# Kernel optimization log

Hardware: AMD Instinct MI355X
Metric: run time of the kernel (lower is better)

The kernel has to match this reference:

```python
import math
import jax, jax.numpy as jnp
import numpy as np

N_HEADS = 32
N_KV_HEADS = 8
HEAD_DIM = 128
DIM = 4096
B = 32
MAX_SEQ = 4096
Q_LEN = 1
START_POS = 4095


def setup_inputs() -> dict:
    key = jax.random.key(0)
    ks = jax.random.split(key, 9)
    x = jax.random.normal(ks[0], (B, Q_LEN, DIM), dtype=jnp.float32)
    # RoPE angles for the current positions (seqlen=Q_LEN, half head_dim pairs)
    inv_freq = 1.0 / (500000.0 ** (np.arange(0, HEAD_DIM, 2, dtype=np.float32) / HEAD_DIM))
    pos = np.arange(START_POS, START_POS + Q_LEN, dtype=np.float32)
    ang = pos[:, None] * inv_freq[None, :]  # [Q_LEN, HEAD_DIM//2]
    freqs_cos = jnp.asarray(np.cos(ang), dtype=jnp.float32)
    freqs_sin = jnp.asarray(np.sin(ang), dtype=jnp.float32)
    cache_k = jax.random.normal(ks[1], (B, MAX_SEQ, N_KV_HEADS, HEAD_DIM), dtype=jnp.float32)
    cache_v = jax.random.normal(ks[2], (B, MAX_SEQ, N_KV_HEADS, HEAD_DIM), dtype=jnp.float32)
    s = 0.02
    wq = jax.random.normal(ks[3], (N_HEADS * HEAD_DIM, DIM), dtype=jnp.float32) * s
    wk = jax.random.normal(ks[4], (N_KV_HEADS * HEAD_DIM, DIM), dtype=jnp.float32) * s
    wv = jax.random.normal(ks[5], (N_KV_HEADS * HEAD_DIM, DIM), dtype=jnp.float32) * s
    wo = jax.random.normal(ks[6], (DIM, N_HEADS * HEAD_DIM), dtype=jnp.float32) * s
    return {"x": x, "start_pos": START_POS, "freqs_cos": freqs_cos, "freqs_sin": freqs_sin,
            "cache_k": cache_k, "cache_v": cache_v, "wq": wq, "wk": wk, "wv": wv, "wo": wo}


def _rope(t, cos, sin):
    # t: [B, S, h, hd]; cos/sin: [S, hd//2]; complex multiply on (even, odd) pairs
    tr = t.reshape(*t.shape[:-1], HEAD_DIM // 2, 2)
    a, b = tr[..., 0], tr[..., 1]
    c = cos[None, :, None, :]
    s = sin[None, :, None, :]
    out = jnp.stack([a * c - b * s, a * s + b * c], axis=-1)
    return out.reshape(t.shape)


def reference(x, start_pos, freqs_cos, freqs_sin, cache_k, cache_v, wq, wk, wv, wo):
    bsz, seqlen, _ = x.shape
    n_rep = N_HEADS // N_KV_HEADS
    xq = jnp.einsum('bsd,od->bso', x, wq).reshape(bsz, seqlen, N_HEADS, HEAD_DIM)
    xk = jnp.einsum('bsd,od->bso', x, wk).reshape(bsz, seqlen, N_KV_HEADS, HEAD_DIM)
    xv = jnp.einsum('bsd,od->bso', x, wv).reshape(bsz, seqlen, N_KV_HEADS, HEAD_DIM)
    xq = _rope(xq, freqs_cos, freqs_sin)
    xk = _rope(xk, freqs_cos, freqs_sin)
    # KV-cache update (start_pos is a static Python int)
    cache_k = cache_k.at[:, start_pos:start_pos + seqlen].set(xk)
    cache_v = cache_v.at[:, start_pos:start_pos + seqlen].set(xv)
    keys = cache_k[:, :start_pos + seqlen]    # [B, T, Hkv, hd]
    values = cache_v[:, :start_pos + seqlen]  # [B, T, Hkv, hd]
    # GQA: group query heads [H] -> [Hkv, n_rep]; avoids materializing repeated KV
    q = xq.reshape(bsz, seqlen, N_KV_HEADS, n_rep, HEAD_DIM)
    scale = 1.0 / math.sqrt(HEAD_DIM)
    scores = jnp.einsum('bsgrd,btgd->bgrst', q, keys) * scale  # [B, Hkv, n_rep, S, T]
    probs = jax.nn.softmax(scores, axis=-1)
    out = jnp.einsum('bgrst,btgd->bsgrd', probs, values)
    out = out.reshape(bsz, seqlen, N_HEADS * HEAD_DIM)
    return jnp.einsum('bse,de->bsd', out, wo)
```

## Files before the change

kernel.cpp:

```cpp
#include <hip/hip_runtime.h>

#define B_    32
#define DIM_  4096
#define NH_   32
#define NKV_  8
#define HD_   128
#define TSEQ  4096
#define NQKV  6144
#define GSPLIT 32
#define BK    32
#define NT    256
#define TSPL  8
#define TS    512

__device__ __forceinline__ const float* wrow(const float* w0, const float* w1,
                                             const float* w2, int b1, int b2, int col) {
    if (col < b1) return w0 + (size_t)col * DIM_;
    if (col < b2) return w1 + (size_t)(col - b1) * DIM_;
    return w2 + (size_t)(col - b2) * DIM_;
}

__global__ __launch_bounds__(128) void gemm32(
    const float* __restrict__ A, const float* __restrict__ w0,
    const float* __restrict__ w1, const float* __restrict__ w2,
    int b1, int b2, int N, float* __restrict__ po)
{
    __shared__ __align__(16) float wt[BK][NT + 4];
    __shared__ __align__(16) float xs[BK][36];
    const int tid = threadIdx.x;
    const int cg  = tid & 31;
    const int bg  = tid >> 5;
    const int ct  = blockIdx.x * NT;
    const int k0  = blockIdx.y * (DIM_ / GSPLIT);

    float acc[8][8];
    #pragma unroll
    for (int i = 0; i < 8; ++i)
        #pragma unroll
        for (int j = 0; j < 8; ++j) acc[i][j] = 0.f;

    const int kq = (tid & 7) * 4;
    const int rr = tid >> 3;

    for (int kt = 0; kt < DIM_ / GSPLIT; kt += BK) {
        const int kb = k0 + kt;
        #pragma unroll
        for (int st = 0; st < 16; ++st) {
            const int c = st * 16 + rr;
            const float* wr = wrow(w0, w1, w2, b1, b2, ct + c);
            const float4 wv = *(const float4*)(wr + kb + kq);
            wt[kq + 0][c] = wv.x; wt[kq + 1][c] = wv.y;
            wt[kq + 2][c] = wv.z; wt[kq + 3][c] = wv.w;
        }
        #pragma unroll
        for (int st = 0; st < 2; ++st) {
            const int b = st * 16 + rr;
            const float4 xv = *(const float4*)(A + (size_t)b * DIM_ + kb + kq);
            xs[kq + 0][b] = xv.x; xs[kq + 1][b] = xv.y;
            xs[kq + 2][b] = xv.z; xs[kq + 3][b] = xv.w;
        }
        __syncthreads();
        #pragma unroll 8
        for (int kk = 0; kk < BK; ++kk) {
            const float4 xa = *(const float4*)&xs[kk][bg * 8];
            const float4 xb = *(const float4*)&xs[kk][bg * 8 + 4];
            const float4 wa = *(const float4*)&wt[kk][cg * 4];
            const float4 wb = *(const float4*)&wt[kk][128 + cg * 4];
            const float xv[8] = {xa.x, xa.y, xa.z, xa.w, xb.x, xb.y, xb.z, xb.w};
            const float wv[8] = {wa.x, wa.y, wa.z, wa.w, wb.x, wb.y, wb.z, wb.w};
            #pragma unroll
            for (int i = 0; i < 8; ++i)
                #pragma unroll
                for (int j = 0; j < 8; ++j)
                    acc[i][j] = fmaf(xv[i], wv[j], acc[i][j]);
        }
        __syncthreads();
    }
    const size_t srow = (size_t)blockIdx.y * B_;
    #pragma unroll
    for (int i = 0; i < 8; ++i) {
        const int b = bg * 8 + i;
        const float4 o0 = make_float4(acc[i][0], acc[i][1], acc[i][2], acc[i][3]);
        const float4 o1 = make_float4(acc[i][4], acc[i][5], acc[i][6], acc[i][7]);
        *(float4*)&po[(srow + b) * N + ct + cg * 4]       = o0;
        *(float4*)&po[(srow + b) * N + ct + 128 + cg * 4] = o1;
    }
}

__global__ void reduce_rope(const float* __restrict__ po,
                            const float* __restrict__ fc, const float* __restrict__ fs,
                            float* __restrict__ qkv)
{
    const int pid = blockIdx.x * 256 + threadIdx.x;
    const int b  = pid / 3072;
    const int c0 = (pid - b * 3072) * 2;
    float v0 = 0.f, v1 = 0.f;
    #pragma unroll
    for (int s = 0; s < GSPLIT; ++s) {
        const float* p = po + ((size_t)s * B_ + b) * NQKV + c0;
        v0 += p[0]; v1 += p[1];
    }
    if (c0 < DIM_ + NKV_ * HD_) {
        const int i = (c0 & 127) >> 1;
        const float c = fc[i], sn = fs[i];
        const float o0 = v0 * c - v1 * sn;
        const float o1 = v0 * sn + v1 * c;
        v0 = o0; v1 = o1;
    }
    qkv[(size_t)b * NQKV + c0]     = v0;
    qkv[(size_t)b * NQKV + c0 + 1] = v1;
}

__global__ __launch_bounds__(256) void attn_partial(
    const float* __restrict__ qkv, const float* __restrict__ ck,
    const float* __restrict__ cv,
    float* __restrict__ po , float* __restrict__ pl )
{
    const int blk = blockIdx.x;
    const int s = blk & (TSPL - 1);
    const int g = (blk / TSPL) & 7;
    const int b = blk / (TSPL * NKV_);
    const int tid    = threadIdx.x;
    const int grp    = tid >> 4;
    const int lane16 = tid & 15;
    const int wv     = tid >> 6;
    const int g4     = (tid >> 4) & 3;
    const int d8     = lane16 * 8;
    const float* qb = qkv + (size_t)b * NQKV;

    float4 qa[4], qc[4];
    #pragma unroll
    for (int h = 0; h < 4; ++h) {
        qa[h] = *(const float4*)(qb + (g * 4 + h) * HD_ + d8);
        qc[h] = *(const float4*)(qb + (g * 4 + h) * HD_ + d8 + 4);
    }

    float acc[4][8];
    #pragma unroll
    for (int h = 0; h < 4; ++h)
        #pragma unroll
        for (int e = 0; e < 8; ++e) acc[h][e] = 0.f;
    float l[4] = {0.f, 0.f, 0.f, 0.f};
    const float scale = 0.08838834764831845f;
    const int t0 = s * TS + grp;

    for (int it = 0; it < TS / 16; ++it) {
        const int t = t0 + it * 16;
        const float *kp, *vp;
        if (t == TSEQ - 1) {
            kp = qb + DIM_ + g * HD_;
            vp = qb + DIM_ + NKV_ * HD_ + g * HD_;
        } else {
            const size_t off = (((size_t)b * TSEQ + t) * NKV_ + g) * HD_;
            kp = ck + off; vp = cv + off;
        }
        const float4 k0 = *(const float4*)(kp + d8);
        const float4 k1 = *(const float4*)(kp + d8 + 4);
        float p[4];
        #pragma unroll
        for (int h = 0; h < 4; ++h) {
            p[h] = k0.x*qa[h].x + k0.y*qa[h].y + k0.z*qa[h].z + k0.w*qa[h].w
                 + k1.x*qc[h].x + k1.y*qc[h].y + k1.z*qc[h].z + k1.w*qc[h].w;
        }
        #pragma unroll
        for (int off = 1; off < 16; off <<= 1) {
            #pragma unroll
            for (int h = 0; h < 4; ++h) p[h] += __shfl_xor(p[h], off);
        }
        #pragma unroll
        for (int h = 0; h < 4; ++h) {
            p[h] = __expf(p[h] * scale);
            l[h] += p[h];
        }
        const float4 v0 = *(const float4*)(vp + d8);
        const float4 v1 = *(const float4*)(vp + d8 + 4);
        #pragma unroll
        for (int h = 0; h < 4; ++h) {
            acc[h][0] += p[h]*v0.x; acc[h][1] += p[h]*v0.y;
            acc[h][2] += p[h]*v0.z; acc[h][3] += p[h]*v0.w;
            acc[h][4] += p[h]*v1.x; acc[h][5] += p[h]*v1.y;
            acc[h][6] += p[h]*v1.z; acc[h][7] += p[h]*v1.w;
        }
    }

    #pragma unroll
    for (int off = 16; off < 64; off <<= 1) {
        #pragma unroll
        for (int h = 0; h < 4; ++h) {
            #pragma unroll
            for (int e = 0; e < 8; ++e) acc[h][e] += __shfl_xor(acc[h][e], off);
            l[h] += __shfl_xor(l[h], off);
        }
    }

    __shared__ __align__(16) float ob[4][4][HD_];
    __shared__ float lb[4][4];
    if (g4 == 0) {
        #pragma unroll
        for (int h = 0; h < 4; ++h)
            #pragma unroll
            for (int e = 0; e < 8; ++e) ob[wv][h][d8 + e] = acc[h][e];
        if (lane16 == 0) {
            #pragma unroll
            for (int h = 0; h < 4; ++h) lb[wv][h] = l[h];
        }
    }
    __syncthreads();
    #pragma unroll
    for (int e = tid; e < 512; e += 256) {
        float sum = 0.f;
        #pragma unroll
        for (int c = 0; c < 4; ++c) sum += ob[c][e >> 7][e & 127];
        po[(size_t)blk * 512 + e] = sum;
    }
    if (tid < 4) {
        float sum = 0.f;
        #pragma unroll
        for (int c = 0; c < 4; ++c) sum += lb[c][tid];
        pl[blk * 4 + tid] = sum;
    }
}

__global__ void attn_combine(const float* __restrict__ po, const float* __restrict__ pl,
                             float* __restrict__ ao)
{
    const int bg  = blockIdx.x;
    const int tid = threadIdx.x;
    const int e0  = tid * 4;
    const int r   = e0 >> 7;
    float4 o = make_float4(0.f, 0.f, 0.f, 0.f);
    float ls = 0.f;
    #pragma unroll
    for (int s = 0; s < TSPL; ++s) {
        const float4 v = *(const float4*)&po[((size_t)bg * TSPL + s) * 512 + e0];
        o.x += v.x; o.y += v.y; o.z += v.z; o.w += v.w;
        ls += pl[(bg * TSPL + s) * 4 + r];
    }
    const float inv = 1.f / ls;
    o.x *= inv; o.y *= inv; o.z *= inv; o.w *= inv;
    const int b = bg >> 3, g = bg & 7;
    *(float4*)&ao[(size_t)b * DIM_ + g * 512 + e0] = o;
}

__global__ void reduce_out(const float* __restrict__ po, float* __restrict__ out)
{
    const int i = blockIdx.x * 256 + threadIdx.x;
    const int b = i >> 12, c = i & 4095;
    float v = 0.f;
    #pragma unroll
    for (int s = 0; s < GSPLIT; ++s) v += po[((size_t)s * B_ + b) * DIM_ + c];
    out[i] = v;
}

extern "C" void kernel_launch(void* const* d_in, const int* in_sizes, int n_in,
                              void* d_out, int out_size, void* d_ws, size_t ws_size,
                              hipStream_t stream)
{
    (void)in_sizes; (void)n_in; (void)out_size; (void)ws_size;
    const float* x  = (const float*)d_in[0];
    const float* fc = (const float*)d_in[2];
    const float* fs = (const float*)d_in[3];
    const float* ck = (const float*)d_in[4];
    const float* cv = (const float*)d_in[5];
    const float* wq = (const float*)d_in[6];
    const float* wk = (const float*)d_in[7];
    const float* wv = (const float*)d_in[8];
    const float* wo = (const float*)d_in[9];
    float* out = (float*)d_out;
    float* ws  = (float*)d_ws;

    float* qkv  = ws;
    float* aout = ws + 196608;
    float* apo  = ws + 327680;
    float* apl  = ws + 1376256;
    float* gp   = ws + 1384448;

    gemm32<<<dim3(NQKV / NT, GSPLIT), 128, 0, stream>>>(
        x, wq, wk, wv, DIM_, DIM_ + NKV_ * HD_, NQKV, gp);
    reduce_rope<<<dim3((B_ * (NQKV / 2)) / 256), 256, 0, stream>>>(gp, fc, fs, qkv);
    attn_partial<<<dim3(B_ * NKV_ * TSPL), 256, 0, stream>>>(qkv, ck, cv, apo, apl);
    attn_combine<<<dim3(B_ * NKV_), 128, 0, stream>>>(apo, apl, aout);
    gemm32<<<dim3(DIM_ / NT, GSPLIT), 128, 0, stream>>>(
        aout, wo, wo, wo, DIM_, DIM_, DIM_, gp);
    reduce_out<<<dim3((B_ * DIM_) / 256), 256, 0, stream>>>(gp, out);
}
```

Baseline: 285.3 us.

## Prefetch weights into registers, nontemporal KV streaming, vectorize reductions

The split-K GEMM now stages its whole 128-wide slice of the activation once in shared memory. It register-prefetches the next weight tile with nontemporal loads while computing the current one, and picks the weight base pointer once per block. Attention switches to 32 lanes per key with one float4 each, software-pipelined nontemporal K/V loads, and no per-iteration branch for the fresh token. The reduce kernels use float4 loads and stores. The aim is better overlap of latency on the bandwidth-bound weight and KV-cache streams, at the cost of more registers and longer shuffle chains in attention.

New measurement: 268.6 us. 5.8% less time.

```diff
diff --git a/kernel.cpp b/kernel.cpp
--- a/kernel.cpp
+++ b/kernel.cpp
@@ -13,11 +13,10 @@
 #define TSPL  8
 #define TS    512
 
-__device__ __forceinline__ const float* wrow(const float* w0, const float* w1,
-                                             const float* w2, int b1, int b2, int col) {
-    if (col < b1) return w0 + (size_t)col * DIM_;
-    if (col < b2) return w1 + (size_t)(col - b1) * DIM_;
-    return w2 + (size_t)(col - b2) * DIM_;
+typedef float f4_t __attribute__((ext_vector_type(4)));
+
+__device__ __forceinline__ f4_t ntl(const float* p) {
+    return __builtin_nontemporal_load((const f4_t*)p);
 }
 
 __global__ __launch_bounds__(128) void gemm32(
@@ -26,48 +25,67 @@
     int b1, int b2, int N, float* __restrict__ po)
 {
     __shared__ __align__(16) float wt[BK][NT + 4];
-    __shared__ __align__(16) float xs[BK][36];
+    __shared__ __align__(16) float xp[128][36];
     const int tid = threadIdx.x;
     const int cg  = tid & 31;
     const int bg  = tid >> 5;
     const int ct  = blockIdx.x * NT;
     const int k0  = blockIdx.y * (DIM_ / GSPLIT);
 
+    const float* wb_; int c0_;
+    if (ct < b1)      { wb_ = w0; c0_ = ct; }
+    else if (ct < b2) { wb_ = w1; c0_ = ct - b1; }
+    else              { wb_ = w2; c0_ = ct - b2; }
+
+    {
+        const int kq = (tid & 31) * 4;
+        const int rr = tid >> 5;
+        #pragma unroll
+        for (int st = 0; st < 8; ++st) {
+            const int bb = st * 4 + rr;
+            const float4 xv = *(const float4*)(A + (size_t)bb * DIM_ + k0 + kq);
+            xp[kq + 0][bb] = xv.x; xp[kq + 1][bb] = xv.y;
+            xp[kq + 2][bb] = xv.z; xp[kq + 3][bb] = xv.w;
+        }
+    }
+
+    const int kq2 = (tid & 7) * 4;
+    const int rr2 = tid >> 3;
+    f4_t wreg[16];
+
+    #pragma unroll
+    for (int st = 0; st < 16; ++st)
+        wreg[st] = ntl(wb_ + (size_t)(c0_ + st * 16 + rr2) * DIM_ + k0 + kq2);
+    #pragma unroll
+    for (int st = 0; st < 16; ++st) {
+        const int c = st * 16 + rr2;
+        wt[kq2 + 0][c] = wreg[st][0]; wt[kq2 + 1][c] = wreg[st][1];
+        wt[kq2 + 2][c] = wreg[st][2]; wt[kq2 + 3][c] = wreg[st][3];
+    }
+    __syncthreads();
+
     float acc[8][8];
     #pragma unroll
     for (int i = 0; i < 8; ++i)
         #pragma unroll
         for (int j = 0; j < 8; ++j) acc[i][j] = 0.f;
 
-    const int kq = (tid & 7) * 4;
-    const int rr = tid >> 3;
-
-    for (int kt = 0; kt < DIM_ / GSPLIT; kt += BK) {
-        const int kb = k0 + kt;
-        #pragma unroll
-        for (int st = 0; st < 16; ++st) {
-            const int c = st * 16 + rr;
-            const float* wr = wrow(w0, w1, w2, b1, b2, ct + c);
-            const float4 wv = *(const float4*)(wr + kb + kq);
-            wt[kq + 0][c] = wv.x; wt[kq + 1][c] = wv.y;
-            wt[kq + 2][c] = wv.z; wt[kq + 3][c] = wv.w;
-        }
-        #pragma unroll
-        for (int st = 0; st < 2; ++st) {
-            const int b = st * 16 + rr;
-            const float4 xv = *(const float4*)(A + (size_t)b * DIM_ + kb + kq);
-            xs[kq + 0][b] = xv.x; xs[kq + 1][b] = xv.y;
-            xs[kq + 2][b] = xv.z; xs[kq + 3][b] = xv.w;
-        }
-        __syncthreads();
+    for (int t = 0; t < 4; ++t) {
+        if (t < 3) {
+            #pragma unroll
+            for (int st = 0; st < 16; ++st)
+                wreg[st] = ntl(wb_ + (size_t)(c0_ + st * 16 + rr2) * DIM_
+                               + k0 + (t + 1) * BK + kq2);
+        }
         #pragma unroll 8
         for (int kk = 0; kk < BK; ++kk) {
-            const float4 xa = *(const float4*)&xs[kk][bg * 8];
-            const float4 xb = *(const float4*)&xs[kk][bg * 8 + 4];
+            const int kr = t * BK + kk;
+            const float4 xa = *(const float4*)&xp[kr][bg * 8];
+            const float4 xb = *(const float4*)&xp[kr][bg * 8 + 4];
             const float4 wa = *(const float4*)&wt[kk][cg * 4];
-            const float4 wb = *(const float4*)&wt[kk][128 + cg * 4];
+            const float4 wb4 = *(const float4*)&wt[kk][128 + cg * 4];
             const float xv[8] = {xa.x, xa.y, xa.z, xa.w, xb.x, xb.y, xb.z, xb.w};
-            const float wv[8] = {wa.x, wa.y, wa.z, wa.w, wb.x, wb.y, wb.z, wb.w};
+            const float wv[8] = {wa.x, wa.y, wa.z, wa.w, wb4.x, wb4.y, wb4.z, wb4.w};
             #pragma unroll
             for (int i = 0; i < 8; ++i)
                 #pragma unroll
@@ -75,7 +93,17 @@
                     acc[i][j] = fmaf(xv[i], wv[j], acc[i][j]);
         }
         __syncthreads();
-    }
+        if (t < 3) {
+            #pragma unroll
+            for (int st = 0; st < 16; ++st) {
+                const int c = st * 16 + rr2;
+                wt[kq2 + 0][c] = wreg[st][0]; wt[kq2 + 1][c] = wreg[st][1];
+                wt[kq2 + 2][c] = wreg[st][2]; wt[kq2 + 3][c] = wreg[st][3];
+            }
+            __syncthreads();
+        }
+    }
+
     const size_t srow = (size_t)blockIdx.y * B_;
     #pragma unroll
     for (int i = 0; i < 8; ++i) {
@@ -92,23 +120,46 @@
                             float* __restrict__ qkv)
 {
     const int pid = blockIdx.x * 256 + threadIdx.x;
-    const int b  = pid / 3072;
-    const int c0 = (pid - b * 3072) * 2;
-    float v0 = 0.f, v1 = 0.f;
-    #pragma unroll
-    for (int s = 0; s < GSPLIT; ++s) {
-        const float* p = po + ((size_t)s * B_ + b) * NQKV + c0;
-        v0 += p[0]; v1 += p[1];
-    }
+    const int b  = pid / (NQKV / 4);
+    const int c0 = (pid - b * (NQKV / 4)) * 4;
+    f4_t v = {0.f, 0.f, 0.f, 0.f};
+    #pragma unroll
+    for (int s = 0; s < GSPLIT; ++s)
+        v += *(const f4_t*)(po + ((size_t)s * B_ + b) * NQKV + c0);
     if (c0 < DIM_ + NKV_ * HD_) {
         const int i = (c0 & 127) >> 1;
-        const float c = fc[i], sn = fs[i];
-        const float o0 = v0 * c - v1 * sn;
-        const float o1 = v0 * sn + v1 * c;
-        v0 = o0; v1 = o1;
-    }
-    qkv[(size_t)b * NQKV + c0]     = v0;
-    qkv[(size_t)b * NQKV + c0 + 1] = v1;
+        const float ca = fc[i],     sa = fs[i];
+        const float cb = fc[i + 1], sb = fs[i + 1];
+        f4_t o;
+        o[0] = v[0] * ca - v[1] * sa;
+        o[1] = v[0] * sa + v[1] * ca;
+        o[2] = v[2] * cb - v[3] * sb;
+        o[3] = v[2] * sb + v[3] * cb;
+        v = o;
+    }
+    *(f4_t*)(qkv + (size_t)b * NQKV + c0) = v;
+}
+
+__device__ __forceinline__ void attn_step(const f4_t kc, const f4_t vc,
+                                          const f4_t* q, f4_t* acc, float* l)
+{
+    float p0 = kc[0]*q[0][0] + kc[1]*q[0][1] + kc[2]*q[0][2] + kc[3]*q[0][3];
+    float p1 = kc[0]*q[1][0] + kc[1]*q[1][1] + kc[2]*q[1][2] + kc[3]*q[1][3];
+    float p2 = kc[0]*q[2][0] + kc[1]*q[2][1] + kc[2]*q[2][2] + kc[3]*q[2][3];
+    float p3 = kc[0]*q[3][0] + kc[1]*q[3][1] + kc[2]*q[3][2] + kc[3]*q[3][3];
+    #pragma unroll
+    for (int off = 1; off < 32; off <<= 1) {
+        p0 += __shfl_xor(p0, off);
+        p1 += __shfl_xor(p1, off);
+        p2 += __shfl_xor(p2, off);
+        p3 += __shfl_xor(p3, off);
+    }
+    const float scale = 0.08838834764831845f;
+    p0 = __expf(p0 * scale); p1 = __expf(p1 * scale);
+    p2 = __expf(p2 * scale); p3 = __expf(p3 * scale);
+    l[0] += p0; l[1] += p1; l[2] += p2; l[3] += p3;
+    acc[0] += p0 * vc; acc[1] += p1 * vc;
+    acc[2] += p2 * vc; acc[3] += p3 * vc;
 }
 
 __global__ __launch_bounds__(256) void attn_partial(
@@ -120,105 +171,72 @@
     const int s = blk & (TSPL - 1);
     const int g = (blk / TSPL) & 7;
     const int b = blk / (TSPL * NKV_);
-    const int tid    = threadIdx.x;
-    const int grp    = tid >> 4;
-    const int lane16 = tid & 15;
-    const int wv     = tid >> 6;
-    const int g4     = (tid >> 4) & 3;
-    const int d8     = lane16 * 8;
+    const int tid  = threadIdx.x;
+    const int grp  = tid >> 5;
+    const int lane = tid & 31;
+    const int wv   = tid >> 6;
+    const int d4   = lane * 4;
     const float* qb = qkv + (size_t)b * NQKV;
 
-    float4 qa[4], qc[4];
+    f4_t q[4];
+    #pragma unroll
+    for (int h = 0; h < 4; ++h)
+        q[h] = *(const f4_t*)(qb + (g * 4 + h) * HD_ + d4);
+
+    f4_t zero4 = {0.f, 0.f, 0.f, 0.f};
+    f4_t acc[4] = {zero4, zero4, zero4, zero4};
+    float l[4] = {0.f, 0.f, 0.f, 0.f};
+
+    const int t0 = s * TS + grp;
+    int niter = TS / 8;
+    const bool fresh = (s == TSPL - 1) && (grp == 7);
+    if (fresh) --niter;
+
+    const size_t base = (((size_t)b * TSEQ + t0) * NKV_ + g) * HD_ + d4;
+    const float* kp = ck + base;
+    const float* vp = cv + base;
+    const size_t step = (size_t)8 * NKV_ * HD_;
+
+    f4_t kc = ntl(kp), vc = ntl(vp);
+    for (int it = 0; it < niter - 1; ++it) {
+        kp += step; vp += step;
+        const f4_t kn = ntl(kp);
+        const f4_t vn = ntl(vp);
+        attn_step(kc, vc, q, acc, l);
+        kc = kn; vc = vn;
+    }
+    attn_step(kc, vc, q, acc, l);
+    if (fresh) {
+        const f4_t kf = *(const f4_t*)(qb + DIM_ + g * HD_ + d4);
+        const f4_t vf = *(const f4_t*)(qb + DIM_ + NKV_ * HD_ + g * HD_ + d4);
+        attn_step(kf, vf, q, acc, l);
+    }
+
     #pragma unroll
     for (int h = 0; h < 4; ++h) {
-        qa[h] = *(const float4*)(qb + (g * 4 + h) * HD_ + d8);
-        qc[h] = *(const float4*)(qb + (g * 4 + h) * HD_ + d8 + 4);
-    }
-
-    float acc[4][8];
-    #pragma unroll
-    for (int h = 0; h < 4; ++h)
         #pragma unroll
-        for (int e = 0; e < 8; ++e) acc[h][e] = 0.f;
-    float l[4] = {0.f, 0.f, 0.f, 0.f};
-    const float scale = 0.08838834764831845f;
-    const int t0 = s * TS + grp;
-
-    for (int it = 0; it < TS / 16; ++it) {
-        const int t = t0 + it * 16;
-        const float *kp, *vp;
-        if (t == TSEQ - 1) {
-            kp = qb + DIM_ + g * HD_;
-            vp = qb + DIM_ + NKV_ * HD_ + g * HD_;
-        } else {
-            const size_t off = (((size_t)b * TSEQ + t) * NKV_ + g) * HD_;
-            kp = ck + off; vp = cv + off;
-        }
-        const float4 k0 = *(const float4*)(kp + d8);
-        const float4 k1 = *(const float4*)(kp + d8 + 4);
-        float p[4];
-        #pragma unroll
-        for (int h = 0; h < 4; ++h) {
-            p[h] = k0.x*qa[h].x + k0.y*qa[h].y + k0.z*qa[h].z + k0.w*qa[h].w
-                 + k1.x*qc[h].x + k1.y*qc[h].y + k1.z*qc[h].z + k1.w*qc[h].w;
-        }
-        #pragma unroll
-        for (int off = 1; off < 16; off <<= 1) {
-            #pragma unroll
-            for (int h = 0; h < 4; ++h) p[h] += __shfl_xor(p[h], off);
-        }
-        #pragma unroll
-        for (int h = 0; h < 4; ++h) {
-            p[h] = __expf(p[h] * scale);
-            l[h] += p[h];
-        }
-        const float4 v0 = *(const float4*)(vp + d8);
-        const float4 v1 = *(const float4*)(vp + d8 + 4);
-        #pragma unroll
-        for (int h = 0; h < 4; ++h) {
-            acc[h][0] += p[h]*v0.x; acc[h][1] += p[h]*v0.y;
-            acc[h][2] += p[h]*v0.z; acc[h][3] += p[h]*v0.w;
-            acc[h][4] += p[h]*v1.x; acc[h][5] += p[h]*v1.y;
-            acc[h][6] += p[h]*v1.z; acc[h][7] += p[h]*v1.w;
-        }
-    }
-
-    #pragma unroll
-    for (int off = 16; off < 64; off <<= 1) {
-        #pragma unroll
-        for (int h = 0; h < 4; ++h) {
-            #pragma unroll
-            for (int e = 0; e < 8; ++e) acc[h][e] += __shfl_xor(acc[h][e], off);
-            l[h] += __shfl_xor(l[h], off);
-        }
+        for (int e = 0; e < 4; ++e) acc[h][e] += __shfl_xor(acc[h][e], 32);
+        l[h] += __shfl_xor(l[h], 32);
     }
 
     __shared__ __align__(16) float ob[4][4][HD_];
     __shared__ float lb[4][4];
-    if (g4 == 0) {
+    if ((tid & 32) == 0) {
         #pragma unroll
-        for (int h = 0; h < 4; ++h)
-            #pragma unroll
-            for (int e = 0; e < 8; ++e) ob[wv][h][d8 + e] = acc[h][e];
-        if (lane16 == 0) {
-            #pragma unroll
-            for (int h = 0; h < 4; ++h) lb[wv][h] = l[h];
+        for (int h = 0; h < 4; ++h) *(f4_t*)&ob[wv][h][d4] = acc[h];
+        if (lane == 0) {
+            lb[wv][0] = l[0]; lb[wv][1] = l[1]; lb[wv][2] = l[2]; lb[wv][3] = l[3];
         }
     }
     __syncthreads();
     #pragma unroll
     for (int e = tid; e < 512; e += 256) {
-        float sum = 0.f;
-        #pragma unroll
-        for (int c = 0; c < 4; ++c) sum += ob[c][e >> 7][e & 127];
+        const float sum = ob[0][e >> 7][e & 127] + ob[1][e >> 7][e & 127]
+                        + ob[2][e >> 7][e & 127] + ob[3][e >> 7][e & 127];
         po[(size_t)blk * 512 + e] = sum;
     }
-    if (tid < 4) {
-        float sum = 0.f;
-        #pragma unroll
-        for (int c = 0; c < 4; ++c) sum += lb[c][tid];
-        pl[blk * 4 + tid] = sum;
-    }
+    if (tid < 4)
+        pl[blk * 4 + tid] = lb[0][tid] + lb[1][tid] + lb[2][tid] + lb[3][tid];
 }
 
 __global__ void attn_combine(const float* __restrict__ po, const float* __restrict__ pl,
@@ -228,28 +246,28 @@
     const int tid = threadIdx.x;
     const int e0  = tid * 4;
     const int r   = e0 >> 7;
-    float4 o = make_float4(0.f, 0.f, 0.f, 0.f);
+    f4_t o = {0.f, 0.f, 0.f, 0.f};
     float ls = 0.f;
     #pragma unroll
     for (int s = 0; s < TSPL; ++s) {
-        const float4 v = *(const float4*)&po[((size_t)bg * TSPL + s) * 512 + e0];
-        o.x += v.x; o.y += v.y; o.z += v.z; o.w += v.w;
+        o += *(const f4_t*)&po[((size_t)bg * TSPL + s) * 512 + e0];
         ls += pl[(bg * TSPL + s) * 4 + r];
     }
-    const float inv = 1.f / ls;
-    o.x *= inv; o.y *= inv; o.z *= inv; o.w *= inv;
+    o *= (1.f / ls);
     const int b = bg >> 3, g = bg & 7;
-    *(float4*)&ao[(size_t)b * DIM_ + g * 512 + e0] = o;
+    *(f4_t*)&ao[(size_t)b * DIM_ + g * 512 + e0] = o;
 }
 
 __global__ void reduce_out(const float* __restrict__ po, float* __restrict__ out)
 {
-    const int i = blockIdx.x * 256 + threadIdx.x;
-    const int b = i >> 12, c = i & 4095;
-    float v = 0.f;
-    #pragma unroll
-    for (int s = 0; s < GSPLIT; ++s) v += po[((size_t)s * B_ + b) * DIM_ + c];
-    out[i] = v;
+    const int pid = blockIdx.x * 256 + threadIdx.x;
+    const int b  = pid >> 10;
+    const int c0 = (pid & 1023) * 4;
+    f4_t v = {0.f, 0.f, 0.f, 0.f};
+    #pragma unroll
+    for (int s = 0; s < GSPLIT; ++s)
+        v += *(const f4_t*)(po + ((size_t)s * B_ + b) * DIM_ + c0);
+    *(f4_t*)(out + (size_t)b * DIM_ + c0) = v;
 }
 
 extern "C" void kernel_launch(void* const* d_in, const int* in_sizes, int n_in,
@@ -277,10 +295,10 @@
 
     gemm32<<<dim3(NQKV / NT, GSPLIT), 128, 0, stream>>>(
         x, wq, wk, wv, DIM_, DIM_ + NKV_ * HD_, NQKV, gp);
-    reduce_rope<<<dim3((B_ * (NQKV / 2)) / 256), 256, 0, stream>>>(gp, fc, fs, qkv);
+    reduce_rope<<<dim3(B_ * (NQKV / 4) / 256), 256, 0, stream>>>(gp, fc, fs, qkv);
     attn_partial<<<dim3(B_ * NKV_ * TSPL), 256, 0, stream>>>(qkv, ck, cv, apo, apl);
     attn_combine<<<dim3(B_ * NKV_), 128, 0, stream>>>(apo, apl, aout);
     gemm32<<<dim3(DIM_ / NT, GSPLIT), 128, 0, stream>>>(
         aout, wo, wo, wo, DIM_, DIM_, DIM_, gp);
-    reduce_out<<<dim3((B_ * DIM_) / 256), 256, 0, stream>>>(gp, out);
-}
+    reduce_out<<<dim3(B_ * DIM_ / 4 / 256), 256, 0, stream>>>(gp, out);
+}
```
